# Kernel optimization log

Hardware: AMD Instinct MI355X
Metric: run time of the kernel (lower is better)

The kernel has to match this reference:

```python
import jax, jax.numpy as jnp
import numpy as np

B, N, DIM, H = 4, 2048, 1024, 16
HEAD_DIM = DIM // H
SCALE = HEAD_DIM ** (-0.5)


def setup_inputs() -> dict:
    key = jax.random.key(0)
    k1, k2, k3 = jax.random.split(key, 3)
    x = jax.random.normal(k1, (B, N, DIM), dtype=jnp.float32)
    # nn.Linear(dim, 3*dim, bias=False): weight shape [3*dim, dim], y = x @ W.T
    w_qkv = jax.random.normal(k2, (3 * DIM, DIM), dtype=jnp.float32) * 0.02
    w_proj = jax.random.normal(k3, (DIM, DIM), dtype=jnp.float32) * 0.02
    return {"x": x, "w_qkv": w_qkv, "w_proj": w_proj}


def reference(x, w_qkv, w_proj):
    Bv, Nv, C = x.shape
    Dh = C // H
    # qkv projection -> [B, N, 3, H, Dh]
    qkv = (x @ w_qkv.T).reshape(Bv, Nv, 3, H, Dh)
    q, k, v = qkv[:, :, 0], qkv[:, :, 1], qkv[:, :, 2]  # each [B, N, H, Dh]
    # scaled dot-product attention per head (online-softmax loop collapses to this)
    scores = jnp.einsum("bnhd,bmhd->bhnm", q, k) * SCALE  # [B, H, N, N]
    attn = jax.nn.softmax(scores, axis=-1)
    out = jnp.einsum("bhnm,bmhd->bnhd", attn, v).reshape(Bv, Nv, C)
    return out @ w_proj.T
```

## Files before the change

### kernel.cpp

```cpp
#include <hip/hip_runtime.h>

typedef __bf16 bf16;
typedef bf16 bf16x8 __attribute__((ext_vector_type(8)));
typedef float f32x4 __attribute__((ext_vector_type(4)));
typedef float f32x16 __attribute__((ext_vector_type(16)));
typedef int i32x2 __attribute__((ext_vector_type(2)));

#define B_   4
#define N_   2048
#define DIM_ 1024
#define H_   16
#define DH_  64
#define M_   (B_ * N_)

#define CEXP 0.18033688f

#define GLOBAL_CP(g) (const __attribute__((address_space(1))) void*)(g)
#define LDS_CP(l)    (__attribute__((address_space(3))) void*)(l)

__global__ __launch_bounds__(256) void cvt_all(
    const float* __restrict__ x, const float* __restrict__ wq,
    const float* __restrict__ wp, bf16* __restrict__ o,
    int nx4, int nwq4, int nwp4)
{
    const int i = blockIdx.x * blockDim.x + threadIdx.x;
    const float* src; int si;
    if (i < nx4)                { src = x;  si = i; }
    else if (i < nx4 + nwq4)    { src = wq; si = i - nx4; }
    else                        { src = wp; si = i - nx4 - nwq4; }
    const float4 v = ((const float4*)src)[si];
    union { bf16 h[4]; uint2 u; } r;
    r.h[0] = (bf16)v.x; r.h[1] = (bf16)v.y;
    r.h[2] = (bf16)v.z; r.h[3] = (bf16)v.w;
    ((uint2*)o)[i] = r.u;
}

__global__ __launch_bounds__(256) void gemm_bt(
    const bf16* __restrict__ A, const bf16* __restrict__ Bm,
    int Ndim, int K, int mode,
    float* __restrict__ outf,
    bf16* __restrict__ qb, bf16* __restrict__ kbv, bf16* __restrict__ vbT)
{
    __shared__ bf16 As[128 * 64];
    __shared__ bf16 Bs[128 * 64];

    const int tid  = threadIdx.x;
    const int wave = tid >> 6;
    const int lane = tid & 63;
    const int quad = lane >> 4;
    const int lr   = lane & 15;
    const int wr   = wave >> 1, wc = wave & 1;
    const int m0 = blockIdx.y * 128;
    const int n0 = blockIdx.x * 128;

    f32x4 acc[4][4];
#pragma unroll
    for (int i = 0; i < 4; i++)
#pragma unroll
        for (int j = 0; j < 4; j++) acc[i][j] = f32x4{0.f, 0.f, 0.f, 0.f};

    const int sl8 = lane >> 3;
    const int sc8 = ((lane & 7) ^ (sl8 & 7)) * 8;

    for (int k0 = 0; k0 < K; k0 += 64) {
        __syncthreads();
#pragma unroll
        for (int c = 0; c < 4; c++) {
            const int ii  = wave * 4 + c;
            const int row = ii * 8 + sl8;
            __builtin_amdgcn_global_load_lds(
                GLOBAL_CP(A + (size_t)(m0 + row) * K + k0 + sc8),
                LDS_CP(&As[ii * 512 + lane * 8]), 16, 0, 0);
            __builtin_amdgcn_global_load_lds(
                GLOBAL_CP(Bm + (size_t)(n0 + row) * K + k0 + sc8),
                LDS_CP(&Bs[ii * 512 + lane * 8]), 16, 0, 0);
        }
        __syncthreads();

#pragma unroll
        for (int s = 0; s < 2; s++) {
            bf16x8 af[4], bfr[4];
#pragma unroll
            for (int i = 0; i < 4; i++) {
                const int R = wr * 64 + i * 16 + lr;
                af[i] = *(const bf16x8*)(&As[R * 64 + (((s * 4 + quad) ^ (R & 7)) << 3)]);
            }
#pragma unroll
            for (int j = 0; j < 4; j++) {
                const int R = wc * 64 + j * 16 + lr;
                bfr[j] = *(const bf16x8*)(&Bs[R * 64 + (((s * 4 + quad) ^ (R & 7)) << 3)]);
            }
#pragma unroll
            for (int i = 0; i < 4; i++)
#pragma unroll
                for (int j = 0; j < 4; j++)
                    acc[i][j] = __builtin_amdgcn_mfma_f32_16x16x32_bf16(
                        af[i], bfr[j], acc[i][j], 0, 0, 0);
        }
    }

#pragma unroll
    for (int i = 0; i < 4; i++) {
        const int mbase = m0 + wr * 64 + i * 16 + quad * 4;
#pragma unroll
        for (int j = 0; j < 4; j++) {
            const int n = n0 + wc * 64 + j * 16 + lr;
            if (mode == 0) {
#pragma unroll
                for (int r = 0; r < 4; r++)
                    outf[(size_t)(mbase + r) * Ndim + n] = acc[i][j][r];
            } else {
                const int which = n >> 10;
                const int h = (n >> 6) & 15;
                const int d = n & 63;
                const int b  = mbase >> 11;
                const int t0 = mbase & 2047;
                if (which == 2) {
                    union { uint2 u; bf16 hh[4]; } p;
#pragma unroll
                    for (int r = 0; r < 4; r++) p.hh[r] = (bf16)acc[i][j][r];
                    *(uint2*)(&vbT[(((size_t)(b * 16 + h)) * 64 + d) * 2048 + t0]) = p.u;
                } else {
                    bf16* dst = (which == 0) ? qb : kbv;
                    const float sc = (which == 0) ? CEXP : 1.0f;
#pragma unroll
                    for (int r = 0; r < 4; r++)
                        dst[(((size_t)(b * 16 + h)) * 2048 + t0 + r) * 64 + d] =
                            (bf16)(acc[i][j][r] * sc);
                }
            }
        }
    }
}

__global__ __launch_bounds__(256, 4) void attn_kernel(
    const bf16* __restrict__ qb, const bf16* __restrict__ kb,
    const bf16* __restrict__ vbT, bf16* __restrict__ ao)
{
    __shared__ bf16 Ks[2][64 * 64];
    __shared__ bf16 Vs[2][64 * 64];

    const int tid  = threadIdx.x;
    const int wave = tid >> 6;
    const int lane = tid & 63;
    const int l31  = lane & 31;
    const int hh   = lane >> 5;

    const int bid = blockIdx.x;
    const int qt  = (bid >> 3) & 15;
    const int bh  = ((bid >> 7) << 3) | (bid & 7);

    const bf16* Q  = qb  + (size_t)bh * N_ * DH_;
    const bf16* Kp = kb  + (size_t)bh * N_ * DH_;
    const bf16* Vp = vbT + (size_t)bh * DH_ * N_;

    bf16x8 qf[4];
#pragma unroll
    for (int ks = 0; ks < 4; ks++)
        qf[ks] = *(const bf16x8*)(Q + (size_t)(qt * 128 + wave * 32 + l31) * DH_
                                    + ks * 16 + hh * 8);

    bf16x8 onesb;
#pragma unroll
    for (int j = 0; j < 8; j++) onesb[j] = (bf16)1.0f;

    const int srow = lane >> 3;
    const int scol = ((lane & 7) ^ (srow & 7)) * 8;

    f32x16 oacc[2];
    f32x16 sacc;
#pragma unroll
    for (int r = 0; r < 16; r++) { oacc[0][r] = 0.f; oacc[1][r] = 0.f; sacc[r] = 0.f; }

#define STAGE(t, pb)                                                          \
    do {                                                                      \
        _Pragma("unroll")                                                     \
        for (int c = 0; c < 2; c++) {                                         \
            const int ii  = wave * 2 + c;                           \
            const int row = ii * 8 + srow;                         \
            __builtin_amdgcn_global_load_lds(                                 \
                GLOBAL_CP(Kp + (size_t)((t) * 64 + row) * DH_ + scol),        \
                LDS_CP(&Ks[pb][ii * 512 + lane * 8]), 16, 0, 0);              \
            __builtin_amdgcn_global_load_lds(                                 \
                GLOBAL_CP(Vp + (size_t)row * N_ + (t) * 64 + scol),           \
                LDS_CP(&Vs[pb][ii * 512 + lane * 8]), 16, 0, 0);              \
        }                                                                     \
    } while (0)

    STAGE(0, 0);
    __syncthreads();

    int cur = 0;
    for (int t = 0; t < N_ / 64; t++) {
        if (t + 1 < N_ / 64) STAGE(t + 1, cur ^ 1);

#pragma unroll
        for (int kbk = 0; kbk < 2; kbk++) {
            f32x16 e;
#pragma unroll
            for (int r = 0; r < 16; r++) e[r] = 0.f;
#pragma unroll
            for (int ks = 0; ks < 4; ks++) {
                const int R  = kbk * 32 + l31;
                const int ch = ks * 2 + hh;
                bf16x8 ak = *(const bf16x8*)(&Ks[cur][R * 64 + ((ch ^ (R & 7)) << 3)]);
                e = __builtin_amdgcn_mfma_f32_32x32x16_bf16(ak, qf[ks], e, 0, 0, 0);
            }

#pragma unroll
            for (int r = 0; r < 16; r++) e[r] = exp2f(e[r]);

            uint g[8];
#pragma unroll
            for (int m = 0; m < 8; m++) {
                union { uint u; bf16 h2[2]; } pk;
                pk.h2[0] = (bf16)e[2 * m];
                pk.h2[1] = (bf16)e[2 * m + 1];
                g[m] = pk.u;
            }

            const i32x2 s0 = __builtin_amdgcn_permlane32_swap((int)g[0], (int)g[2], false, false);
            const i32x2 s1 = __builtin_amdgcn_permlane32_swap((int)g[1], (int)g[3], false, false);
            const i32x2 s2 = __builtin_amdgcn_permlane32_swap((int)g[4], (int)g[6], false, false);
            const i32x2 s3 = __builtin_amdgcn_permlane32_swap((int)g[5], (int)g[7], false, false);

            union { uint u[4]; bf16x8 v; } p0u, p1u;
            p0u.u[0] = (uint)s0[0];
            p0u.u[1] = (uint)s1[0];
            p0u.u[2] = (uint)s0[1];
            p0u.u[3] = (uint)s1[1];
            p1u.u[0] = (uint)s2[0];
            p1u.u[1] = (uint)s3[0];
            p1u.u[2] = (uint)s2[1];
            p1u.u[3] = (uint)s3[1];

            sacc = __builtin_amdgcn_mfma_f32_32x32x16_bf16(p0u.v, onesb, sacc, 0, 0, 0);
            sacc = __builtin_amdgcn_mfma_f32_32x32x16_bf16(p1u.v, onesb, sacc, 0, 0, 0);

#pragma unroll
            for (int dblk = 0; dblk < 2; dblk++) {
                const int R   = dblk * 32 + l31;
                const int ch0 = kbk * 4 + hh;
                const int ch1 = kbk * 4 + 2 + hh;
                bf16x8 bv0 = *(const bf16x8*)(&Vs[cur][R * 64 + ((ch0 ^ (R & 7)) << 3)]);
                bf16x8 bv1 = *(const bf16x8*)(&Vs[cur][R * 64 + ((ch1 ^ (R & 7)) << 3)]);
                oacc[dblk] = __builtin_amdgcn_mfma_f32_32x32x16_bf16(p0u.v, bv0, oacc[dblk], 0, 0, 0);
                oacc[dblk] = __builtin_amdgcn_mfma_f32_32x32x16_bf16(p1u.v, bv1, oacc[dblk], 0, 0, 0);
            }
        }

        __syncthreads();
        cur ^= 1;
    }
#undef STAGE

    const int head = bh & 15;
    const int b    = bh >> 4;
#pragma unroll
    for (int r = 0; r < 16; r++) {
        const int qr  = (r & 3) + 8 * (r >> 2) + 4 * hh;
        const float inv = 1.0f / sacc[r];
        const int qrow = qt * 128 + wave * 32 + qr;
#pragma unroll
        for (int dblk = 0; dblk < 2; dblk++)
            ao[((size_t)(b * 2048 + qrow)) * 1024 + head * 64 + dblk * 32 + l31] =
                (bf16)(oacc[dblk][r] * inv);
    }
}

extern "C" void kernel_launch(void* const* d_in, const int* in_sizes, int n_in,
                              void* d_out, int out_size, void* d_ws, size_t ws_size,
                              hipStream_t stream)
{
    const float* x     = (const float*)d_in[0];
    const float* wqkv  = (const float*)d_in[1];
    const float* wproj = (const float*)d_in[2];
    float* out = (float*)d_out;

    const size_t nx  = (size_t)M_ * DIM_;
    const size_t nwq = (size_t)3 * DIM_ * DIM_;
    const size_t nwp = (size_t)DIM_ * DIM_;
    const size_t seg = (size_t)B_ * H_ * N_ * DH_;

    bf16* xb     = (bf16*)d_ws;
    bf16* wqkvb  = xb + nx;
    bf16* wprojb = wqkvb + nwq;
    bf16* qb     = wprojb + nwp;
    bf16* kb     = qb + seg;
    bf16* vbT    = kb + seg;
    bf16* ao     = xb;

    const int nx4  = (int)(nx / 4), nwq4 = (int)(nwq / 4), nwp4 = (int)(nwp / 4);
    cvt_all<<<(nx4 + nwq4 + nwp4) / 256, 256, 0, stream>>>(
        x, wqkv, wproj, xb, nx4, nwq4, nwp4);

    gemm_bt<<<dim3(24, 64), 256, 0, stream>>>(xb, wqkvb, 3 * DIM_, DIM_, 1,
                                              nullptr, qb, kb, vbT);
    attn_kernel<<<dim3(1024), 256, 0, stream>>>(qb, kb, vbT, ao);
    gemm_bt<<<dim3(8, 64), 256, 0, stream>>>(ao, wprojb, DIM_, DIM_, 0,
                                             out, nullptr, nullptr, nullptr);
}
```

Measured before the change: 299.7 us.

## Repack attention K/V tiles into 128-wide swizzled LDS rows, hoist V loads, add setprio

Changes the shared-memory layout of K and V tiles from 64x64 with an 8-way XOR swizzle to 32x128 rows (two logical rows per physical row) with a 16-way XOR swizzle, adjusting both the global-to-LDS staging and the fragment reads. It also hoists the V fragment LDS reads ahead of the exp/pack stage so they overlap the softmax math, and wraps the MFMA sections in s_setprio to favour matrix issue across waves. The aim is fewer LDS bank conflicts and better latency hiding, at the cost of more address arithmetic and extra live registers for the hoisted V fragments.

```diff
diff --git a/kernel.cpp b/kernel.cpp
--- a/kernel.cpp
+++ b/kernel.cpp
@@ -137,8 +137,8 @@
     const bf16* __restrict__ qb, const bf16* __restrict__ kb,
     const bf16* __restrict__ vbT, bf16* __restrict__ ao)
 {
-    __shared__ bf16 Ks[2][64 * 64];
-    __shared__ bf16 Vs[2][64 * 64];
+    __shared__ bf16 Ks[2][32 * 128];
+    __shared__ bf16 Vs[2][32 * 128];
 
     const int tid  = threadIdx.x;
     const int wave = tid >> 6;
@@ -164,8 +164,8 @@
 #pragma unroll
     for (int j = 0; j < 8; j++) onesb[j] = (bf16)1.0f;
 
-    const int srow = lane >> 3;
-    const int scol = ((lane & 7) ^ (srow & 7)) * 8;
+    const int sr = lane >> 4;
+    const int sp = lane & 15;
 
     f32x16 oacc[2];
     f32x16 sacc;
@@ -175,14 +175,17 @@
 #define STAGE(t, pb)                                                          \
     do {                                                                      \
         _Pragma("unroll")                                                     \
-        for (int c = 0; c < 2; c++) {                                         \
-            const int ii  = wave * 2 + c;                           \
-            const int row = ii * 8 + srow;                         \
+        for (int c2 = 0; c2 < 2; c2++) {                                      \
+            const int ii = wave * 2 + c2;                           \
+            const int rr = ii * 4 + sr;                            \
+            const int lc = sp ^ (rr & 15);                 \
+            const int kk = 2 * rr + (lc >> 3);           \
+            const int d0 = (lc & 7) * 8;               \
             __builtin_amdgcn_global_load_lds(                                 \
-                GLOBAL_CP(Kp + (size_t)((t) * 64 + row) * DH_ + scol),        \
+                GLOBAL_CP(Kp + (size_t)((t) * 64 + kk) * DH_ + d0),           \
                 LDS_CP(&Ks[pb][ii * 512 + lane * 8]), 16, 0, 0);              \
             __builtin_amdgcn_global_load_lds(                                 \
-                GLOBAL_CP(Vp + (size_t)row * N_ + (t) * 64 + scol),           \
+                GLOBAL_CP(Vp + (size_t)kk * N_ + (t) * 64 + d0),              \
                 LDS_CP(&Vs[pb][ii * 512 + lane * 8]), 16, 0, 0);              \
         }                                                                     \
     } while (0)
@@ -199,12 +202,29 @@
             f32x16 e;
 #pragma unroll
             for (int r = 0; r < 16; r++) e[r] = 0.f;
+            __builtin_amdgcn_s_setprio(1);
 #pragma unroll
             for (int ks = 0; ks < 4; ks++) {
                 const int R  = kbk * 32 + l31;
+                const int rr = R >> 1;
                 const int ch = ks * 2 + hh;
-                bf16x8 ak = *(const bf16x8*)(&Ks[cur][R * 64 + ((ch ^ (R & 7)) << 3)]);
+                const int pc = (((R & 1) << 3) | ch) ^ (rr & 15);
+                bf16x8 ak = *(const bf16x8*)(&Ks[cur][rr * 128 + pc * 8]);
                 e = __builtin_amdgcn_mfma_f32_32x32x16_bf16(ak, qf[ks], e, 0, 0, 0);
+            }
+            __builtin_amdgcn_s_setprio(0);
+
+            bf16x8 bv[2][2];
+#pragma unroll
+            for (int dblk = 0; dblk < 2; dblk++) {
+#pragma unroll
+                for (int half = 0; half < 2; half++) {
+                    const int Rv  = dblk * 32 + l31;
+                    const int rv  = Rv >> 1;
+                    const int chv = kbk * 4 + half * 2 + hh;
+                    const int pv_ = (((Rv & 1) << 3) | chv) ^ (rv & 15);
+                    bv[dblk][half] = *(const bf16x8*)(&Vs[cur][rv * 128 + pv_ * 8]);
+                }
             }
 
 #pragma unroll
@@ -234,19 +254,16 @@
             p1u.u[2] = (uint)s2[1];
             p1u.u[3] = (uint)s3[1];
 
+            __builtin_amdgcn_s_setprio(1);
             sacc = __builtin_amdgcn_mfma_f32_32x32x16_bf16(p0u.v, onesb, sacc, 0, 0, 0);
             sacc = __builtin_amdgcn_mfma_f32_32x32x16_bf16(p1u.v, onesb, sacc, 0, 0, 0);
 
 #pragma unroll
             for (int dblk = 0; dblk < 2; dblk++) {
-                const int R   = dblk * 32 + l31;
-                const int ch0 = kbk * 4 + hh;
-                const int ch1 = kbk * 4 + 2 + hh;
-                bf16x8 bv0 = *(const bf16x8*)(&Vs[cur][R * 64 + ((ch0 ^ (R & 7)) << 3)]);
-                bf16x8 bv1 = *(const bf16x8*)(&Vs[cur][R * 64 + ((ch1 ^ (R & 7)) << 3)]);
-                oacc[dblk] = __builtin_amdgcn_mfma_f32_32x32x16_bf16(p0u.v, bv0, oacc[dblk], 0, 0, 0);
-                oacc[dblk] = __builtin_amdgcn_mfma_f32_32x32x16_bf16(p1u.v, bv1, oacc[dblk], 0, 0, 0);
-            }
+                oacc[dblk] = __builtin_amdgcn_mfma_f32_32x32x16_bf16(p0u.v, bv[dblk][0], oacc[dblk], 0, 0, 0);
+                oacc[dblk] = __builtin_amdgcn_mfma_f32_32x32x16_bf16(p1u.v, bv[dblk][1], oacc[dblk], 0, 0, 0);
+            }
+            __builtin_amdgcn_s_setprio(0);
         }
 
         __syncthreads();
```

After: 301.4 us. No clear change (+0.6%).
